# Performance work log

Measured on AMD Instinct MI355X. Metric: run time of the kernel, lower is better.

Reference implementation:

```python
import jax, jax.numpy as jnp
import numpy as np

D_MODEL = 1024
D_STATE = 16
D_CONV = 4
EXPAND = 2
D_INNER = EXPAND * D_MODEL          # 2048
DT_RANK = (D_MODEL + 15) // 16      # 64
BATCH = 1
SEQLEN = 1024


def setup_inputs() -> dict:
    key = jax.random.key(0)
    ks = jax.random.split(key, 9)
    s = 0.02  # weight scale for numerical stability
    x = jax.random.normal(ks[0], (BATCH, SEQLEN, D_MODEL), jnp.float32)
    W_in = jax.random.normal(ks[1], (2 * D_INNER, D_MODEL), jnp.float32) * s
    conv_w = jax.random.normal(ks[2], (D_INNER, D_CONV), jnp.float32) * 0.1
    conv_b = jax.random.normal(ks[3], (D_INNER,), jnp.float32) * 0.1
    W_xproj = jax.random.normal(ks[4], (DT_RANK + 2 * D_STATE, D_INNER), jnp.float32) * s
    W_dt = jax.random.normal(ks[5], (D_INNER, DT_RANK), jnp.float32) * s
    b_dt = jax.random.normal(ks[6], (D_INNER,), jnp.float32) * 0.1
    # official init: A = repeat(arange(1, d_state+1), 'n -> d n'); A_log = log(A)
    A_log = jnp.log(jnp.tile(jnp.arange(1, D_STATE + 1, dtype=jnp.float32), (D_INNER, 1)))
    D_skip = jnp.ones((D_INNER,), jnp.float32)
    W_out = jax.random.normal(ks[7], (D_MODEL, D_INNER), jnp.float32) * s
    return {"x": x, "W_in": W_in, "conv_w": conv_w, "conv_b": conv_b,
            "W_xproj": W_xproj, "W_dt": W_dt, "b_dt": b_dt,
            "A_log": A_log, "D_skip": D_skip, "W_out": W_out}


def _mamba_fwd(x, W_in, conv_w, conv_b, W_xproj, W_dt, b_dt, A_log, D_skip, W_out):
    B, L, _ = x.shape
    # input projection -> (B, L, 2*d_inner), split into x-branch and gate z
    xz = x @ W_in.T
    xi, z = jnp.split(xz, 2, axis=-1)
    # causal depthwise conv1d over length
    xc = jnp.transpose(xi, (0, 2, 1))  # (B, d_inner, L)
    xc = jax.lax.conv_general_dilated(
        xc, conv_w[:, None, :], window_strides=(1,),
        padding=[(D_CONV - 1, 0)], feature_group_count=D_INNER)
    xc = jax.nn.silu(xc + conv_b[None, :, None])
    xi = jnp.transpose(xc, (0, 2, 1))  # (B, L, d_inner)
    # data-dependent SSM parameters
    x_dbl = xi @ W_xproj.T  # (B, L, dt_rank + 2*d_state)
    dt, Bm, Cm = jnp.split(x_dbl, [DT_RANK, DT_RANK + D_STATE], axis=-1)
    delta = jax.nn.softplus(dt @ W_dt.T + b_dt)  # (B, L, d_inner)
    A = -jnp.exp(A_log)  # (d_inner, d_state)
    # discretize: h_t = exp(delta*A) * h_{t-1} + (delta*x) * B_t
    deltaA = jnp.exp(jnp.einsum('bld,dn->bldn', delta, A))          # (B,L,d,n)
    deltaBx = jnp.einsum('bld,bln->bldn', delta * xi, Bm)            # (B,L,d,n)

    def step(h, inp):
        dA_t, dBx_t, c_t = inp
        h = dA_t * h + dBx_t                    # (B, d_inner, d_state)
        y = jnp.einsum('bdn,bn->bd', h, c_t)    # (B, d_inner)
        return h, y

    h0 = jnp.zeros((B, D_INNER, D_STATE), x.dtype)
    _, ys = jax.lax.scan(step, h0, (jnp.transpose(deltaA, (1, 0, 2, 3)),
                                    jnp.transpose(deltaBx, (1, 0, 2, 3)),
                                    jnp.transpose(Cm, (1, 0, 2))))
    y = jnp.transpose(ys, (1, 0, 2))  # (B, L, d_inner)
    y = y + xi * D_skip
    y = y * jax.nn.silu(z)
    return y @ W_out.T  # (B, L, d_model)


def reference(x, W_in, conv_w, conv_b, W_xproj, W_dt, b_dt, A_log, D_skip, W_out):
    return _mamba_fwd(x, W_in, conv_w, conv_b, W_xproj, W_dt, b_dt, A_log, D_skip, W_out)
```

## Files before the change

### kernel.cpp

```cpp
#include <hip/hip_runtime.h>
#include <hip/hip_bf16.h>
#include <math.h>

namespace {

constexpr int SEQ    = 1024;
constexpr int DMODEL = 1024;
constexpr int DINNER = 2048;
constexpr int DSTATE = 16;
constexpr int DTRANK = 64;
constexpr int XPW    = 96;
constexpr int XPWP   = 128;

typedef __attribute__((ext_vector_type(8))) short short8;
typedef __attribute__((ext_vector_type(4))) short short4_t;
typedef __attribute__((ext_vector_type(4))) float floatx4;

#define GLB __attribute__((address_space(1)))
#define LDSAS __attribute__((address_space(3)))

__device__ __forceinline__ float siluf(float x) { return x / (1.f + __expf(-x)); }

__device__ __forceinline__ unsigned short f2b(float f) {
    __hip_bfloat16 h = __float2bfloat16(f);
    return *reinterpret_cast<unsigned short*>(&h);
}
__device__ __forceinline__ float b2f(unsigned short u) {
    union { unsigned int i; float f; } v; v.i = (unsigned int)u << 16; return v.f;
}

constexpr size_t N_XB   = (size_t)SEQ * DMODEL;
constexpr size_t N_WIN  = (size_t)2 * DINNER * DMODEL;
constexpr size_t N_WXP  = (size_t)XPWP * DINNER;
constexpr size_t N_WDT  = (size_t)DINNER * DTRANK;
constexpr size_t N_WOUT = (size_t)DMODEL * DINNER;
constexpr size_t CO1 = N_XB, CO2 = CO1 + N_WIN, CO3 = CO2 + N_WXP,
                 CO4 = CO3 + N_WDT, CO5 = CO4 + N_WOUT;

__global__ __launch_bounds__(256)
void cast_all(const float* __restrict__ x, const float* __restrict__ Win,
              const float* __restrict__ Wxp, const float* __restrict__ Wdt,
              const float* __restrict__ Wout, unsigned short* __restrict__ dst)
{
    size_t i = ((size_t)blockIdx.x * 256 + threadIdx.x) * 8;
    if (i >= CO5) return;
    const float* src; size_t si;
    if (i < CO1)      { src = x;   si = i; }
    else if (i < CO2) { src = Win; si = i - CO1; }
    else if (i < CO3) {
        size_t j = i - CO2, row = j / DINNER;
        if (row >= XPW) { short8 z = {0,0,0,0,0,0,0,0};
                          *reinterpret_cast<short8*>(&dst[i]) = z; return; }
        src = Wxp; si = j;
    }
    else if (i < CO4) { src = Wdt;  si = i - CO3; }
    else              { src = Wout; si = i - CO4; }
    float4 a = *reinterpret_cast<const float4*>(&src[si]);
    float4 b = *reinterpret_cast<const float4*>(&src[si + 4]);
    short8 o;
    o[0]=(short)f2b(a.x); o[1]=(short)f2b(a.y); o[2]=(short)f2b(a.z); o[3]=(short)f2b(a.w);
    o[4]=(short)f2b(b.x); o[5]=(short)f2b(b.y); o[6]=(short)f2b(b.z); o[7]=(short)f2b(b.w);
    *reinterpret_cast<short8*>(&dst[i]) = o;
}

template<int EPI>
__global__ __launch_bounds__(256)
void gemm_mfma(const unsigned short* __restrict__ A, int lda,
               const unsigned short* __restrict__ B, int ldb,
               float* __restrict__ C, int ldc, size_t czstride,
               const float* __restrict__ bias, int Ksub, int nbx,
               unsigned short* __restrict__ gz)
{
    constexpr int BM = 64, BN = 128, BK = 32, MR = 2, NR = 4;
    __shared__ unsigned short Alds[2][BM * BK];
    __shared__ unsigned short Blds[2][BN * BK];

    const int nwg = gridDim.x;
    int id = blockIdx.x;
    int wg = ((nwg & 7) == 0) ? (id & 7) * (nwg >> 3) + (id >> 3) : id;
    const int bx = wg % nbx, by = wg / nbx;

    const int tid  = threadIdx.x;
    const int lane = tid & 63;
    const int wv   = tid >> 6;
    const int wm   = wv >> 1, wn = wv & 1;
    const int fr   = lane & 15;
    const int kg   = lane >> 4;
    const int m0   = by * BM;
    const int n0   = bx * BN;
    const int kb   = blockIdx.z * Ksub;
    const int srow = tid >> 2;
    const int scol = (tid & 3) * 8;
    float* Cz = C + (size_t)blockIdx.z * czstride;

    floatx4 acc[MR][NR];
#pragma unroll
    for (int mi = 0; mi < MR; ++mi)
#pragma unroll
        for (int ni = 0; ni < NR; ++ni)
            acc[mi][ni] = (floatx4){0.f, 0.f, 0.f, 0.f};

    auto stage = [&](int buf, int k0) {
        __builtin_amdgcn_global_load_lds(
            (const GLB unsigned int*)&A[(size_t)(m0 + srow) * lda + k0 + scol],
            (LDSAS unsigned int*)&Alds[buf][tid * 8], 16, 0, 0);
#pragma unroll
        for (int r = 0; r < 2; ++r)
            __builtin_amdgcn_global_load_lds(
                (const GLB unsigned int*)&B[(size_t)(n0 + r * 64 + srow) * ldb + k0 + scol],
                (LDSAS unsigned int*)&Blds[buf][r * 2048 + tid * 8], 16, 0, 0);
    };

    const int nt = Ksub / BK;
    stage(0, kb);
    __syncthreads();
    int cur = 0;
    for (int t = 0; t < nt; ++t) {
        if (t + 1 < nt) stage(cur ^ 1, kb + (t + 1) * BK);
        short8 af[MR], bf[NR];
#pragma unroll
        for (int mi = 0; mi < MR; ++mi)
            af[mi] = *reinterpret_cast<const short8*>(
                &Alds[cur][(wm * 32 + mi * 16 + fr) * BK + kg * 8]);
#pragma unroll
        for (int ni = 0; ni < NR; ++ni)
            bf[ni] = *reinterpret_cast<const short8*>(
                &Blds[cur][(wn * 64 + ni * 16 + fr) * BK + kg * 8]);
#pragma unroll
        for (int mi = 0; mi < MR; ++mi)
#pragma unroll
            for (int ni = 0; ni < NR; ++ni)
                acc[mi][ni] = __builtin_amdgcn_mfma_f32_16x16x32_bf16(
                    af[mi], bf[ni], acc[mi][ni], 0, 0, 0);
        __syncthreads();
        cur ^= 1;
    }

#pragma unroll
    for (int mi = 0; mi < MR; ++mi)
#pragma unroll
        for (int ni = 0; ni < NR; ++ni)
#pragma unroll
            for (int r = 0; r < 4; ++r) {
                int row = m0 + wm * 32 + mi * 16 + kg * 4 + r;
                int col = n0 + wn * 64 + ni * 16 + fr;
                float v = acc[mi][ni][r];
                if constexpr (EPI == 1) {
                    v += bias[col];
                    v = (v > 20.f) ? v : log1pf(__expf(v));
                    Cz[(size_t)row * ldc + col] = v;
                } else if constexpr (EPI == 3) {
                    if (col < DINNER)
                        Cz[(size_t)row * ldc + col] = v;
                    else
                        gz[(size_t)row * DINNER + col - DINNER] = f2b(siluf(v));
                } else {
                    Cz[(size_t)row * ldc + col] = v;
                }
            }
}

__global__ __launch_bounds__(256)
void combine_xdbl(const float* __restrict__ xp, float* __restrict__ xf,
                  unsigned short* __restrict__ xb)
{
    int i = (blockIdx.x * 256 + threadIdx.x) * 4;
    constexpr size_t SL = (size_t)SEQ * XPWP;
    float4 s{0.f, 0.f, 0.f, 0.f};
#pragma unroll
    for (int z = 0; z < 8; ++z) {
        float4 p = *reinterpret_cast<const float4*>(&xp[z * SL + i]);
        s.x += p.x; s.y += p.y; s.z += p.z; s.w += p.w;
    }
    *reinterpret_cast<float4*>(&xf[i]) = s;
    short4_t o; o[0]=(short)f2b(s.x); o[1]=(short)f2b(s.y);
                o[2]=(short)f2b(s.z); o[3]=(short)f2b(s.w);
    *reinterpret_cast<short4_t*>(&xb[i]) = o;
}

__global__ __launch_bounds__(256)
void combine_out(const float* __restrict__ op, float* __restrict__ out)
{
    int i = (blockIdx.x * 256 + threadIdx.x) * 4;
    constexpr size_t SL = (size_t)SEQ * DMODEL;
    float4 s0 = *reinterpret_cast<const float4*>(&op[i]);
    float4 s1 = *reinterpret_cast<const float4*>(&op[SL + i]);
    float4 s2 = *reinterpret_cast<const float4*>(&op[2 * SL + i]);
    float4 s3 = *reinterpret_cast<const float4*>(&op[3 * SL + i]);
    float4 s{ s0.x+s1.x+s2.x+s3.x, s0.y+s1.y+s2.y+s3.y,
              s0.z+s1.z+s2.z+s3.z, s0.w+s1.w+s2.w+s3.w };
    *reinterpret_cast<float4*>(&out[i]) = s;
}

__global__ __launch_bounds__(256)
void conv_silu(const float* __restrict__ xi,
               const float* __restrict__ conv_w,
               const float* __restrict__ conv_b,
               unsigned short* __restrict__ xic)
{
    int idx = blockIdx.x * 256 + threadIdx.x;
    int l0 = (idx / DINNER) * 4;
    int d  = idx % DINNER;
    float4 w = *reinterpret_cast<const float4*>(&conv_w[d * 4]);
    float cb = conv_b[d];
    float v[7];
#pragma unroll
    for (int k = 0; k < 7; ++k) {
        int ls = l0 - 3 + k;
        v[k] = (ls >= 0) ? xi[(size_t)ls * DINNER + d] : 0.f;
    }
#pragma unroll
    for (int j = 0; j < 4; ++j) {
        float acc = cb;
        acc = fmaf(v[j],     w.x, acc);
        acc = fmaf(v[j + 1], w.y, acc);
        acc = fmaf(v[j + 2], w.z, acc);
        acc = fmaf(v[j + 3], w.w, acc);
        xic[(size_t)(l0 + j) * DINNER + d] = f2b(siluf(acc));
    }
}


__global__ __launch_bounds__(256)
void scan_pass1(const float* __restrict__ delta,
                const unsigned short* __restrict__ xic,
                const float* __restrict__ xdbl,
                const float* __restrict__ A_log,
                float* __restrict__ sdlbuf,
                float* __restrict__ Sbuf, int CH)
{
    const int tid = threadIdx.x;
    const int d   = blockIdx.x * 256 + tid;
    const int c   = blockIdx.y;
    const int tb  = c * CH;

    float An[16], h[16];
#pragma unroll
    for (int n = 0; n < 16; ++n) {
        An[n] = -__expf(A_log[(size_t)d * 16 + n]);
        h[n]  = 0.f;
    }
    float sdl = 0.f;

#pragma unroll 4
    for (int t = tb; t < tb + CH; ++t) {
        float dl = delta[(size_t)t * DINNER + d];
        float xv = b2f(xic[(size_t)t * DINNER + d]);
        const float4* R = reinterpret_cast<const float4*>(&xdbl[(size_t)t * XPWP + DTRANK]);
        float4 B0 = R[0], B1 = R[1], B2 = R[2], B3 = R[3];
        float Bv[16] = {B0.x,B0.y,B0.z,B0.w, B1.x,B1.y,B1.z,B1.w,
                        B2.x,B2.y,B2.z,B2.w, B3.x,B3.y,B3.z,B3.w};
        float t1 = dl * xv;
        sdl += dl;
#pragma unroll
        for (int n = 0; n < 16; ++n) {
            float a = __expf(dl * An[n]);
            h[n] = fmaf(a, h[n], t1 * Bv[n]);
        }
    }
    sdlbuf[(size_t)c * DINNER + d] = sdl;
#pragma unroll
    for (int n = 0; n < 16; ++n)
        Sbuf[((size_t)c * 16 + n) * DINNER + d] = h[n];
}

__global__ __launch_bounds__(256)
void scan_pass2(const float* __restrict__ sdlbuf,
                const float* __restrict__ A_log,
                float* __restrict__ Sbuf, int NCr)
{
    int idx = blockIdx.x * 256 + threadIdx.x;
    int n = idx >> 11, d = idx & 2047;
    const float Aneg = -__expf(A_log[(size_t)d * 16 + n]);
    float h = 0.f;
    for (int c = 0; c < NCr; ++c) {
        size_t o = (size_t)c * (DINNER * DSTATE) + idx;
        float p = __expf(sdlbuf[(size_t)c * DINNER + d] * Aneg);
        float s = Sbuf[o];
        Sbuf[o] = h;
        h = fmaf(p, h, s);
    }
}

__global__ __launch_bounds__(256)
void scan_pass3(const float* __restrict__ delta,
                const unsigned short* __restrict__ xic,
                const float* __restrict__ xdbl,
                const float* __restrict__ A_log,
                const float* __restrict__ D_skip,
                const unsigned short* __restrict__ gz,
                const float* __restrict__ Hin,
                unsigned short* __restrict__ yfin, int CH)
{
    const int tid = threadIdx.x;
    const int d   = blockIdx.x * 256 + tid;
    const int c   = blockIdx.y;
    const int tb  = c * CH;

    float An[16], h[16];
#pragma unroll
    for (int n = 0; n < 16; ++n) {
        An[n] = -__expf(A_log[(size_t)d * 16 + n]);
        h[n]  = Hin[((size_t)c * 16 + n) * DINNER + d];
    }
    const float Dsk = D_skip[d];

#pragma unroll 4
    for (int t = tb; t < tb + CH; ++t) {
        float dl = delta[(size_t)t * DINNER + d];
        float xv = b2f(xic[(size_t)t * DINNER + d]);
        float zv = b2f(gz[(size_t)t * DINNER + d]);
        const float4* R = reinterpret_cast<const float4*>(&xdbl[(size_t)t * XPWP + DTRANK]);
        float4 B0 = R[0], B1 = R[1], B2 = R[2], B3 = R[3];
        float4 C0 = R[4], C1 = R[5], C2 = R[6], C3 = R[7];
        float Bv[16] = {B0.x,B0.y,B0.z,B0.w, B1.x,B1.y,B1.z,B1.w,
                        B2.x,B2.y,B2.z,B2.w, B3.x,B3.y,B3.z,B3.w};
        float Cv[16] = {C0.x,C0.y,C0.z,C0.w, C1.x,C1.y,C1.z,C1.w,
                        C2.x,C2.y,C2.z,C2.w, C3.x,C3.y,C3.z,C3.w};
        float t1 = dl * xv;
        float y = 0.f;
#pragma unroll
        for (int n = 0; n < 16; ++n) {
            float a = __expf(dl * An[n]);
            h[n] = fmaf(a, h[n], t1 * Bv[n]);
            y = fmaf(h[n], Cv[n], y);
        }
        float yv = fmaf(xv, Dsk, y) * zv;
        yfin[(size_t)t * DINNER + d] = f2b(yv);
    }
}

}

extern "C" void kernel_launch(void* const* d_in, const int* in_sizes, int n_in,
                              void* d_out, int out_size, void* d_ws, size_t ws_size,
                              hipStream_t stream)
{
    (void)in_sizes; (void)n_in; (void)out_size;

    const float* x       = (const float*)d_in[0];
    const float* W_in    = (const float*)d_in[1];
    const float* conv_w  = (const float*)d_in[2];
    const float* conv_b  = (const float*)d_in[3];
    const float* W_xproj = (const float*)d_in[4];
    const float* W_dt    = (const float*)d_in[5];
    const float* b_dt    = (const float*)d_in[6];
    const float* A_log   = (const float*)d_in[7];
    const float* D_skip  = (const float*)d_in[8];
    const float* W_out   = (const float*)d_in[9];
    float* out = (float*)d_out;

    const size_t F32_FIXED = 2 * (size_t)SEQ * DINNER
                           + (size_t)SEQ * XPWP
                           + 8 * (size_t)SEQ * XPWP;
    const size_t BF16_SHORTS = CO5 + 3 * (size_t)SEQ * DINNER + (size_t)SEQ * XPWP;
    auto need = [&](int nc) {
        return (F32_FIXED + (size_t)nc * DINNER + (size_t)nc * DINNER * DSTATE) * 4
             + BF16_SHORTS * 2;
    };
    int NC = 64;
    if (need(64) > ws_size) NC = 32;
    if (need(32) > ws_size) NC = 16;
    const int CH = SEQ / NC;

    float* ws     = (float*)d_ws;
    float* xi_f   = ws;
    float* delta  = xi_f   + (size_t)SEQ * DINNER;
    float* xdbl_f = delta  + (size_t)SEQ * DINNER;
    float* xpart  = xdbl_f + (size_t)SEQ * XPWP;
    float* sdlbuf = xpart  + 8 * (size_t)SEQ * XPWP;
    float* Sbuf   = sdlbuf + (size_t)NC * DINNER;
    unsigned short* x_b    = (unsigned short*)(Sbuf + (size_t)NC * DINNER * DSTATE);
    unsigned short* Win_b  = x_b + CO1;
    unsigned short* Wxp_b  = x_b + CO2;
    unsigned short* Wdt_b  = x_b + CO3;
    unsigned short* Wout_b = x_b + CO4;
    unsigned short* xic_b  = x_b + CO5;
    unsigned short* yfin_b = xic_b  + (size_t)SEQ * DINNER;
    unsigned short* gz_b   = yfin_b + (size_t)SEQ * DINNER;
    unsigned short* xdbl_b = gz_b   + (size_t)SEQ * DINNER;
    float* opart = xi_f;

    cast_all<<<(int)((CO5 / 8 + 255) / 256), 256, 0, stream>>>(
        x, W_in, W_xproj, W_dt, W_out, x_b);

    gemm_mfma<3><<<dim3(512, 1, 1), 256, 0, stream>>>(
        x_b, DMODEL, Win_b, DMODEL, xi_f, DINNER, 0, nullptr, DMODEL, 32, gz_b);

    conv_silu<<<(SEQ / 4) * DINNER / 256, 256, 0, stream>>>(xi_f, conv_w, conv_b, xic_b);

    gemm_mfma<0><<<dim3(16, 1, 8), 256, 0, stream>>>(
        xic_b, DINNER, Wxp_b, DINNER, xpart, XPWP, (size_t)SEQ * XPWP,
        nullptr, DINNER / 8, 1, nullptr);
    combine_xdbl<<<(SEQ * XPWP) / 1024, 256, 0, stream>>>(xpart, xdbl_f, xdbl_b);

    gemm_mfma<1><<<dim3(256, 1, 1), 256, 0, stream>>>(
        xdbl_b, XPWP, Wdt_b, DTRANK, delta, DINNER, 0, b_dt, DTRANK, 16, nullptr);

    scan_pass1<<<dim3(DINNER / 256, NC), 256, 0, stream>>>(
        delta, xic_b, xdbl_f, A_log, sdlbuf, Sbuf, CH);
    scan_pass2<<<(DINNER * DSTATE) / 256, 256, 0, stream>>>(sdlbuf, A_log, Sbuf, NC);
    scan_pass3<<<dim3(DINNER / 256, NC), 256, 0, stream>>>(
        delta, xic_b, xdbl_f, A_log, D_skip, gz_b, Sbuf, yfin_b, CH);

    gemm_mfma<0><<<dim3(128, 1, 4), 256, 0, stream>>>(
        yfin_b, DINNER, Wout_b, DINNER, opart, DMODEL, (size_t)SEQ * DMODEL,
        nullptr, DINNER / 4, 8, nullptr);
    combine_out<<<(SEQ * DMODEL) / 1024, 256, 0, stream>>>(opart, out);
}
```

Measured before the change: 117.7 us.

## Double GEMM K-tile with XOR-swizzled LDS layout; shrink scan_pass2 blocks

The MFMA GEMM K-tile grows from 32 to 64. Each stage now issues more global-to-LDS loads, and an XOR swizzle on the 16-byte column slot spreads fragment reads across LDS banks, aiming to cut both sync overhead per K and bank conflicts. scan_pass2 moves to 64-thread blocks so its sequential chunk recurrence spreads over more CUs. The out-projection partials get their own workspace buffer instead of aliasing xi_f, which needs more workspace. LDS per block doubles and fewer K iterations remain for pipelining on split-K GEMMs.

```diff
diff --git a/kernel.cpp b/kernel.cpp
--- a/kernel.cpp
+++ b/kernel.cpp
@@ -71,7 +71,7 @@
                const float* __restrict__ bias, int Ksub, int nbx,
                unsigned short* __restrict__ gz)
 {
-    constexpr int BM = 64, BN = 128, BK = 32, MR = 2, NR = 4;
+    constexpr int BM = 64, BN = 128, BK = 64, MR = 2, NR = 4;
     __shared__ unsigned short Alds[2][BM * BK];
     __shared__ unsigned short Blds[2][BN * BK];
 
@@ -89,9 +89,11 @@
     const int m0   = by * BM;
     const int n0   = bx * BN;
     const int kb   = blockIdx.z * Ksub;
-    const int srow = tid >> 2;
-    const int scol = (tid & 3) * 8;
     float* Cz = C + (size_t)blockIdx.z * czstride;
+
+    const int srow = tid >> 3;
+    const int uslt = tid & 7;
+    const int fsw  = fr & 7;
 
     floatx4 acc[MR][NR];
 #pragma unroll
@@ -101,14 +103,22 @@
             acc[mi][ni] = (floatx4){0.f, 0.f, 0.f, 0.f};
 
     auto stage = [&](int buf, int k0) {
-        __builtin_amdgcn_global_load_lds(
-            (const GLB unsigned int*)&A[(size_t)(m0 + srow) * lda + k0 + scol],
-            (LDSAS unsigned int*)&Alds[buf][tid * 8], 16, 0, 0);
-#pragma unroll
-        for (int r = 0; r < 2; ++r)
+#pragma unroll
+        for (int r = 0; r < 2; ++r) {
+            int row = r * 32 + srow;
+            int gc  = k0 + ((uslt ^ (row & 7)) << 3);
             __builtin_amdgcn_global_load_lds(
-                (const GLB unsigned int*)&B[(size_t)(n0 + r * 64 + srow) * ldb + k0 + scol],
+                (const GLB unsigned int*)&A[(size_t)(m0 + row) * lda + gc],
+                (LDSAS unsigned int*)&Alds[buf][r * 2048 + tid * 8], 16, 0, 0);
+        }
+#pragma unroll
+        for (int r = 0; r < 4; ++r) {
+            int row = r * 32 + srow;
+            int gc  = k0 + ((uslt ^ (row & 7)) << 3);
+            __builtin_amdgcn_global_load_lds(
+                (const GLB unsigned int*)&B[(size_t)(n0 + row) * ldb + gc],
                 (LDSAS unsigned int*)&Blds[buf][r * 2048 + tid * 8], 16, 0, 0);
+        }
     };
 
     const int nt = Ksub / BK;
@@ -117,21 +127,32 @@
     int cur = 0;
     for (int t = 0; t < nt; ++t) {
         if (t + 1 < nt) stage(cur ^ 1, kb + (t + 1) * BK);
-        short8 af[MR], bf[NR];
-#pragma unroll
-        for (int mi = 0; mi < MR; ++mi)
-            af[mi] = *reinterpret_cast<const short8*>(
-                &Alds[cur][(wm * 32 + mi * 16 + fr) * BK + kg * 8]);
-#pragma unroll
-        for (int ni = 0; ni < NR; ++ni)
-            bf[ni] = *reinterpret_cast<const short8*>(
-                &Blds[cur][(wn * 64 + ni * 16 + fr) * BK + kg * 8]);
-#pragma unroll
-        for (int mi = 0; mi < MR; ++mi)
-#pragma unroll
-            for (int ni = 0; ni < NR; ++ni)
-                acc[mi][ni] = __builtin_amdgcn_mfma_f32_16x16x32_bf16(
-                    af[mi], bf[ni], acc[mi][ni], 0, 0, 0);
+        short8 af[2][MR], bf[2][NR];
+#pragma unroll
+        for (int kk = 0; kk < 2; ++kk) {
+#pragma unroll
+            for (int mi = 0; mi < MR; ++mi) {
+                int row = wm * 32 + mi * 16 + fr;
+                int u   = (kk * 4 + kg) ^ fsw;
+                af[kk][mi] = *reinterpret_cast<const short8*>(
+                    &Alds[cur][row * BK + u * 8]);
+            }
+#pragma unroll
+            for (int ni = 0; ni < NR; ++ni) {
+                int row = wn * 64 + ni * 16 + fr;
+                int u   = (kk * 4 + kg) ^ fsw;
+                bf[kk][ni] = *reinterpret_cast<const short8*>(
+                    &Blds[cur][row * BK + u * 8]);
+            }
+        }
+#pragma unroll
+        for (int kk = 0; kk < 2; ++kk)
+#pragma unroll
+            for (int mi = 0; mi < MR; ++mi)
+#pragma unroll
+                for (int ni = 0; ni < NR; ++ni)
+                    acc[mi][ni] = __builtin_amdgcn_mfma_f32_16x16x32_bf16(
+                        af[kk][mi], bf[kk][ni], acc[mi][ni], 0, 0, 0);
         __syncthreads();
         cur ^= 1;
     }
@@ -220,7 +241,6 @@
     }
 }
 
-
 __global__ __launch_bounds__(256)
 void scan_pass1(const float* __restrict__ delta,
                 const unsigned short* __restrict__ xic,
@@ -264,12 +284,12 @@
         Sbuf[((size_t)c * 16 + n) * DINNER + d] = h[n];
 }
 
-__global__ __launch_bounds__(256)
+__global__ __launch_bounds__(64)
 void scan_pass2(const float* __restrict__ sdlbuf,
                 const float* __restrict__ A_log,
                 float* __restrict__ Sbuf, int NCr)
 {
-    int idx = blockIdx.x * 256 + threadIdx.x;
+    int idx = blockIdx.x * 64 + threadIdx.x;
     int n = idx >> 11, d = idx & 2047;
     const float Aneg = -__expf(A_log[(size_t)d * 16 + n]);
     float h = 0.f;
@@ -352,7 +372,8 @@
 
     const size_t F32_FIXED = 2 * (size_t)SEQ * DINNER
                            + (size_t)SEQ * XPWP
-                           + 8 * (size_t)SEQ * XPWP;
+                           + 8 * (size_t)SEQ * XPWP
+                           + 4 * (size_t)SEQ * DMODEL;
     const size_t BF16_SHORTS = CO5 + 3 * (size_t)SEQ * DINNER + (size_t)SEQ * XPWP;
     auto need = [&](int nc) {
         return (F32_FIXED + (size_t)nc * DINNER + (size_t)nc * DINNER * DSTATE) * 4
@@ -368,7 +389,8 @@
     float* delta  = xi_f   + (size_t)SEQ * DINNER;
     float* xdbl_f = delta  + (size_t)SEQ * DINNER;
     float* xpart  = xdbl_f + (size_t)SEQ * XPWP;
-    float* sdlbuf = xpart  + 8 * (size_t)SEQ * XPWP;
+    float* opart  = xpart  + 8 * (size_t)SEQ * XPWP;
+    float* sdlbuf = opart  + 4 * (size_t)SEQ * DMODEL;
     float* Sbuf   = sdlbuf + (size_t)NC * DINNER;
     unsigned short* x_b    = (unsigned short*)(Sbuf + (size_t)NC * DINNER * DSTATE);
     unsigned short* Win_b  = x_b + CO1;
@@ -379,7 +401,6 @@
     unsigned short* yfin_b = xic_b  + (size_t)SEQ * DINNER;
     unsigned short* gz_b   = yfin_b + (size_t)SEQ * DINNER;
     unsigned short* xdbl_b = gz_b   + (size_t)SEQ * DINNER;
-    float* opart = xi_f;
 
     cast_all<<<(int)((CO5 / 8 + 255) / 256), 256, 0, stream>>>(
         x, W_in, W_xproj, W_dt, W_out, x_b);
@@ -399,7 +420,7 @@
 
     scan_pass1<<<dim3(DINNER / 256, NC), 256, 0, stream>>>(
         delta, xic_b, xdbl_f, A_log, sdlbuf, Sbuf, CH);
-    scan_pass2<<<(DINNER * DSTATE) / 256, 256, 0, stream>>>(sdlbuf, A_log, Sbuf, NC);
+    scan_pass2<<<(DINNER * DSTATE) / 64, 64, 0, stream>>>(sdlbuf, A_log, Sbuf, NC);
     scan_pass3<<<dim3(DINNER / 256, NC), 256, 0, stream>>>(
         delta, xic_b, xdbl_f, A_log, D_skip, gz_b, Sbuf, yfin_b, CH);
 
```

New measurement: 113.8 us. -3.3%, faster.
